# Performance work log

Measured on AMD Instinct MI355X. Metric: run time of the kernel, lower is better.

## Reference

```python
import jax, jax.numpy as jnp
import numpy as np

D_MODEL = 1024
NUM_HEADS = 16
D_K = D_MODEL // NUM_HEADS
THETA = 10000.0
MAX_SEQ_LEN = 4096


def setup_inputs() -> dict:
    key = jax.random.key(0)
    ks = jax.random.split(key, 5)
    scale = 1.0 / np.sqrt(D_MODEL)
    x = jax.random.normal(ks[0], (2, 2048, D_MODEL), dtype=jnp.float32)
    wq = jax.random.normal(ks[1], (D_MODEL, D_MODEL), dtype=jnp.float32) * scale
    wk = jax.random.normal(ks[2], (D_MODEL, D_MODEL), dtype=jnp.float32) * scale
    wv = jax.random.normal(ks[3], (D_MODEL, D_MODEL), dtype=jnp.float32) * scale
    wo = jax.random.normal(ks[4], (D_MODEL, D_MODEL), dtype=jnp.float32) * scale
    return {"x": x, "wq": wq, "wk": wk, "wv": wv, "wo": wo}


def _rope(t, cos, sin):
    # t: (B, H, S, d_k) with interleaved even/odd pairs
    pairs = t.reshape(*t.shape[:-1], D_K // 2, 2)
    e, o = pairs[..., 0], pairs[..., 1]
    oe = e * cos - o * sin
    oo = e * sin + o * cos
    return jnp.stack([oe, oo], axis=-1).reshape(t.shape)


def reference(x, wq, wk, wv, wo):
    B, S, _ = x.shape
    # QKV projections (Linear: y = x @ W^T, no bias)
    def proj(w):
        y = jnp.einsum('bsd,ed->bse', x, w)
        return y.reshape(B, S, NUM_HEADS, D_K).transpose(0, 2, 1, 3)  # (B,H,S,dk)
    q, k, v = proj(wq), proj(wk), proj(wv)

    # RoPE angles for positions 0..S-1
    pair_idx = jnp.arange(0, D_K, 2, dtype=jnp.float32)
    inv_freq = 1.0 / (THETA ** (pair_idx / D_K))
    pos = jnp.arange(S, dtype=jnp.float32)
    ang = pos[:, None] * inv_freq[None, :]          # (S, dk/2)
    cos, sin = jnp.cos(ang), jnp.sin(ang)
    q = _rope(q, cos, sin)
    k = _rope(k, cos, sin)

    scores = jnp.einsum('bhqd,bhkd->bhqk', q, k) / jnp.sqrt(jnp.float32(D_K))
    causal = jnp.tril(jnp.ones((S, S), dtype=bool))
    scores = jnp.where(causal, scores, jnp.finfo(scores.dtype).min)
    attn = jax.nn.softmax(scores, axis=-1)
    out = jnp.einsum('bhqk,bhkd->bhqd', attn, v)    # (B,H,S,dk)
    out = out.transpose(0, 2, 1, 3).reshape(B, S, D_MODEL)
    return jnp.einsum('bsd,ed->bse', out, wo)
```

## Files before the change

kernel.cpp:

```cpp
#include <hip/hip_runtime.h>
#include <hip/hip_bf16.h>
#include <stdint.h>

#define S_LEN  2048
#define DMODEL 1024
#define NHEADS 16
#define DKH    64
#define NBATCH 2
#define NROWS  (NBATCH * S_LEN)
#define NBH    (NBATCH * NHEADS)
#define KVS    72

typedef unsigned short ushort_t;
typedef __attribute__((ext_vector_type(8))) short bf16x8;
typedef __attribute__((ext_vector_type(4))) float f32x4;
typedef __attribute__((ext_vector_type(4))) unsigned short us4;
typedef __attribute__((ext_vector_type(4))) unsigned int u32x4;

__device__ __forceinline__ ushort_t f2bf(float f) {
  union { float f; unsigned int u; } c; c.f = f;
  unsigned int r = c.u + 0x7FFFu + ((c.u >> 16) & 1u);
  return (ushort_t)(r >> 16);
}

__device__ __forceinline__ unsigned int pack_bf16(float lo, float hi) {
  union { __hip_bfloat162 h; unsigned int u; } cv;
  cv.h = __float22bfloat162_rn(make_float2(lo, hi));
  return cv.u;
}

__device__ __forceinline__ void gload_lds16(const void* g, void* l) {
  __builtin_amdgcn_global_load_lds((const __attribute__((address_space(1))) void*)g,
                                   (__attribute__((address_space(3))) void*)l, 16, 0, 0);
}

__global__ void cast5_kernel(const float* __restrict__ x,
                             const float* __restrict__ a, const float* __restrict__ b,
                             const float* __restrict__ c, const float* __restrict__ d,
                             ushort_t* __restrict__ dst) {
  const int i = (blockIdx.x * 256 + threadIdx.x) * 4;
  const int sel = i >> 20;
  const float* src;
  int off;
  if (sel < 4)      { src = x; off = i; }
  else if (sel == 4){ src = a; off = i & ((1 << 20) - 1); }
  else if (sel == 5){ src = b; off = i & ((1 << 20) - 1); }
  else if (sel == 6){ src = c; off = i & ((1 << 20) - 1); }
  else              { src = d; off = i & ((1 << 20) - 1); }
  const float4 v = *(const float4*)(src + off);
  us4 o;
  o.x = f2bf(v.x); o.y = f2bf(v.y); o.z = f2bf(v.z); o.w = f2bf(v.w);
  *(us4*)(dst + i) = o;
}

template<int EPI>
__device__ __forceinline__ void gemm_core(const ushort_t* __restrict__ A, const ushort_t* __restrict__ Bm,
                                          void* __restrict__ Cp, void* __restrict__ Cp2,
                                          int N, int r0, int c0,
                                          ushort_t* As, ushort_t* Bs)
{
  const int tid  = threadIdx.x;
  const int lane = tid & 63;
  const int w    = tid >> 6;
  const int wr   = (w >> 1) * 64;
  const int wc   = (w & 1) * 64;
  const int g    = lane >> 4;
  const int lr   = lane & 15;
  const int K    = 1024;

  f32x4 acc[4][4] = {};

  const int idx0 = tid, idx1 = 256 + tid;
  const int row0 = idx0 >> 2, ce0 = (idx0 & 3) * 8;
  const int row1 = idx1 >> 2, ce1 = (idx1 & 3) * 8;

  for (int k0 = 0; k0 < K; k0 += 32) {
    gload_lds16(A  + (size_t)(r0 + row0) * K + k0 + ce0, As + idx0 * 8);
    gload_lds16(A  + (size_t)(r0 + row1) * K + k0 + ce1, As + idx1 * 8);
    gload_lds16(Bm + (size_t)(c0 + row0) * K + k0 + ce0, Bs + idx0 * 8);
    gload_lds16(Bm + (size_t)(c0 + row1) * K + k0 + ce1, Bs + idx1 * 8);
    __syncthreads();
    bf16x8 af[4], bfr[4];
    #pragma unroll
    for (int i = 0; i < 4; i++) {
      af[i]  = *(const bf16x8*)(As + (wr + i * 16 + lr) * 32 + g * 8);
      bfr[i] = *(const bf16x8*)(Bs + (wc + i * 16 + lr) * 32 + g * 8);
    }
    #pragma unroll
    for (int mf = 0; mf < 4; mf++)
      #pragma unroll
      for (int nf = 0; nf < 4; nf++)
        acc[mf][nf] = __builtin_amdgcn_mfma_f32_16x16x32_bf16(af[mf], bfr[nf], acc[mf][nf], 0, 0, 0);
    __syncthreads();
  }

  #pragma unroll
  for (int mf = 0; mf < 4; mf++) {
    #pragma unroll
    for (int nf = 0; nf < 4; nf++) {
      #pragma unroll
      for (int r = 0; r < 4; r++) {
        const int row = r0 + wr + mf * 16 + g * 4 + r;
        const int col = c0 + wc + nf * 16 + lr;
        float v = acc[mf][nf][r];
        if constexpr (EPI == 0) {
          ((ushort_t*)Cp)[(size_t)row * N + col] = f2bf(v);
        } else {
          float pv = __shfl_xor(v, 1);
          const int cc  = col & (DMODEL - 1);
          const int pos = row & (S_LEN - 1);
          const int d   = cc & (DKH - 1);
          const int pr  = d >> 1;
          const float inv = exp2f((float)pr * -0.41524100952f);
          const float ang = (float)pos * inv;
          float sn, cs;
          __sincosf(ang, &sn, &cs);
          float outv = (d & 1) ? (pv * sn + v * cs) : (v * cs - pv * sn);
          if (col < DMODEL) outv *= 0.125f;
          const int b = row >> 11, s = row & (S_LEN - 1);
          const int h = cc >> 6;
          ushort_t* dst = (ushort_t*)((col < DMODEL) ? Cp : Cp2);
          dst[(((size_t)(b * NHEADS + h)) * S_LEN + s) * DKH + d] = f2bf(outv);
        }
      }
    }
  }
}

__global__ __launch_bounds__(256, 2)
void proj_kernel(const ushort_t* __restrict__ xb, const ushort_t* __restrict__ wqb,
                 const ushort_t* __restrict__ wvb,
                 ushort_t* __restrict__ qb, ushort_t* __restrict__ kb, ushort_t* __restrict__ vtb)
{
  __shared__ ushort_t As[128 * 32];
  __shared__ ushort_t Bs[128 * 32];
  const int lin = (int)blockIdx.x;
  const int nl  = (lin & 7) * 96 + (lin >> 3);
  if (nl < 512) {
    gemm_core<2>(xb, wqb, qb, kb, 2 * DMODEL, (nl >> 4) * 128, (nl & 15) * 128, As, Bs);
  } else {
    const int m = nl - 512;
    gemm_core<0>(wvb, xb, vtb, nullptr, NROWS, (m >> 5) * 128, (m & 31) * 128, As, Bs);
  }
}

__global__ __launch_bounds__(256, 2)
void gemm_final(const ushort_t* __restrict__ A, const ushort_t* __restrict__ Bm,
                float* __restrict__ Cp)
{
  __shared__ ushort_t As[128 * 32];
  __shared__ ushort_t Bs[64 * 32];
  const int lin  = (int)blockIdx.x;
  const int nl   = (lin & 7) * 64 + (lin >> 3);
  const int r0   = (nl >> 4) * 128;
  const int c0   = (nl & 15) * 64;
  const int tid  = threadIdx.x;
  const int lane = tid & 63;
  const int w    = tid >> 6;
  const int wr   = (w >> 1) * 64;
  const int wc   = (w & 1) * 32;
  const int g    = lane >> 4;
  const int lr   = lane & 15;
  const int K    = 1024;

  f32x4 acc[4][2] = {};
  const int idx0 = tid, idx1 = 256 + tid;
  const int rowA0 = idx0 >> 2, ceA0 = (idx0 & 3) * 8;
  const int rowA1 = idx1 >> 2, ceA1 = (idx1 & 3) * 8;
  const int rowB  = tid >> 2,  ceB  = (tid & 3) * 8;

  for (int k0 = 0; k0 < K; k0 += 32) {
    gload_lds16(A  + (size_t)(r0 + rowA0) * K + k0 + ceA0, As + idx0 * 8);
    gload_lds16(A  + (size_t)(r0 + rowA1) * K + k0 + ceA1, As + idx1 * 8);
    gload_lds16(Bm + (size_t)(c0 + rowB) * K + k0 + ceB,  Bs + tid * 8);
    __syncthreads();
    bf16x8 af[4], bfr[2];
    #pragma unroll
    for (int i = 0; i < 4; i++)
      af[i] = *(const bf16x8*)(As + (wr + i * 16 + lr) * 32 + g * 8);
    #pragma unroll
    for (int i = 0; i < 2; i++)
      bfr[i] = *(const bf16x8*)(Bs + (wc + i * 16 + lr) * 32 + g * 8);
    #pragma unroll
    for (int mf = 0; mf < 4; mf++)
      #pragma unroll
      for (int nf = 0; nf < 2; nf++)
        acc[mf][nf] = __builtin_amdgcn_mfma_f32_16x16x32_bf16(af[mf], bfr[nf], acc[mf][nf], 0, 0, 0);
    __syncthreads();
  }
  #pragma unroll
  for (int mf = 0; mf < 4; mf++)
    #pragma unroll
    for (int nf = 0; nf < 2; nf++)
      #pragma unroll
      for (int r = 0; r < 4; r++) {
        const int row = r0 + wr + mf * 16 + g * 4 + r;
        const int col = c0 + wc + nf * 16 + lr;
        Cp[(size_t)row * DMODEL + col] = acc[mf][nf][r];
      }
}

__global__ __launch_bounds__(512, 4)
void attn_kernel(const ushort_t* __restrict__ Q, const ushort_t* __restrict__ Kh,
                 const ushort_t* __restrict__ VT, ushort_t* __restrict__ Out)
{
  __shared__ ushort_t Ks[2][64 * KVS];
  __shared__ ushort_t Vs[2][64 * KVS];
  const int tid  = threadIdx.x;
  const int lane = tid & 63;
  const int w    = tid >> 6;
  const int grp  = w >> 2;
  const int wid  = w & 3;
  const int g    = lane >> 4, lr = lane & 15;

  const int id = (int)blockIdx.x;
  const int bh = id & 31;
  const int qt = 31 - (id >> 5);
  const int b  = bh >> 4, h = bh & 15;

  const ushort_t* Kbase = Kh + (size_t)bh * S_LEN * DKH;
  const ushort_t* Vbase = VT + (size_t)h * DKH * (size_t)NROWS + (size_t)b * S_LEN;

  ushort_t* Ksg = &Ks[grp][0];
  ushort_t* Vsg = &Vs[grp][0];
  float* MB = (float*)&Ks[1][0];
  float* SB = MB + 64 * 68;

  const int tg   = tid & 255;
  const int krow = tg >> 3;
  const int kcol = (tg & 7) * 8;

  const int qrow = qt * 64 + wid * 16;

  bf16x8 qf0, qf1;
  {
    const ushort_t* qp = Q + ((size_t)bh * S_LEN + qrow + lr) * DKH;
    qf0 = *(const bf16x8*)(qp + g * 8);
    qf1 = *(const bf16x8*)(qp + 32 + g * 8);
  }
  f32x4 o[4] = {};
  float lsum = 0.f;

  bf16x8 kr0, kr1, vr0, vr1;
  if (grp <= qt) {
    const int kv0 = grp * 64;
    kr0 = *(const bf16x8*)(Kbase + (size_t)(kv0 + krow) * DKH + kcol);
    kr1 = *(const bf16x8*)(Kbase + (size_t)(kv0 + 32 + krow) * DKH + kcol);
    vr0 = *(const bf16x8*)(Vbase + (size_t)krow * NROWS + kv0 + kcol);
    vr1 = *(const bf16x8*)(Vbase + (size_t)(32 + krow) * NROWS + kv0 + kcol);
  }

  const int nT = qt / 2 + 1;
  for (int t = 0; t < nT; t++) {
    const int tk  = 2 * t + grp;
    const bool act = (tk <= qt);
    const bool pre = (tk + 2 <= qt);

    __syncthreads();
    if (act) {
      *(bf16x8*)(Ksg + krow * KVS + kcol) = kr0;
      *(bf16x8*)(Ksg + (32 + krow) * KVS + kcol) = kr1;
      *(bf16x8*)(Vsg + krow * KVS + kcol) = vr0;
      *(bf16x8*)(Vsg + (32 + krow) * KVS + kcol) = vr1;
    }
    __syncthreads();
    if (pre) {
      const int kv0n = (tk + 2) * 64;
      kr0 = *(const bf16x8*)(Kbase + (size_t)(kv0n + krow) * DKH + kcol);
      kr1 = *(const bf16x8*)(Kbase + (size_t)(kv0n + 32 + krow) * DKH + kcol);
      vr0 = *(const bf16x8*)(Vbase + (size_t)krow * NROWS + kv0n + kcol);
      vr1 = *(const bf16x8*)(Vbase + (size_t)(32 + krow) * NROWS + kv0n + kcol);
    }

    if (act) {
      f32x4 s4[4];
      __builtin_amdgcn_s_setprio(1);
      #pragma unroll
      for (int nf = 0; nf < 4; nf++) {
        bf16x8 b0 = *(const bf16x8*)(Ksg + (nf * 16 + lr) * KVS + g * 8);
        bf16x8 b1 = *(const bf16x8*)(Ksg + (nf * 16 + lr) * KVS + 32 + g * 8);
        f32x4 z = {};
        z = __builtin_amdgcn_mfma_f32_16x16x32_bf16(b0, qf0, z, 0, 0, 0);
        z = __builtin_amdgcn_mfma_f32_16x16x32_bf16(b1, qf1, z, 0, 0, 0);
        s4[nf] = z;
      }
      __builtin_amdgcn_s_setprio(0);

      if (tk == qt) {
        const int qg = qrow + lr;
        #pragma unroll
        for (int nf = 0; nf < 4; nf++) {
          const int kvb = tk * 64 + nf * 16 + g * 4;
          #pragma unroll
          for (int r = 0; r < 4; r++)
            if (kvb + r > qg) s4[nf][r] = -3.0e38f;
        }
      }

      float p[4][4];
      #pragma unroll
      for (int nf = 0; nf < 4; nf++)
        #pragma unroll
        for (int r = 0; r < 4; r++) p[nf][r] = __expf(s4[nf][r]);
      lsum += ((p[0][0] + p[0][1]) + (p[0][2] + p[0][3])) + ((p[1][0] + p[1][1]) + (p[1][2] + p[1][3]))
            + ((p[2][0] + p[2][1]) + (p[2][2] + p[2][3])) + ((p[3][0] + p[3][1]) + (p[3][2] + p[3][3]));

      bf16x8 pa[2];
      const int src0 = ((g & 1) << 5) + lr;
      const int src1 = src0 + 16;
      const bool xl = (g < 2);
      #pragma unroll
      for (int kf = 0; kf < 2; kf++) {
        const unsigned int x0 = pack_bf16(p[2 * kf][0], p[2 * kf][1]);
        const unsigned int x1 = pack_bf16(p[2 * kf][2], p[2 * kf][3]);
        const unsigned int y0 = pack_bf16(p[2 * kf + 1][0], p[2 * kf + 1][1]);
        const unsigned int y1 = pack_bf16(p[2 * kf + 1][2], p[2 * kf + 1][3]);
        const unsigned int a0 = (unsigned int)__shfl((int)x0, src0);
        const unsigned int b0 = (unsigned int)__shfl((int)y0, src0);
        const unsigned int a1 = (unsigned int)__shfl((int)x1, src0);
        const unsigned int b1 = (unsigned int)__shfl((int)y1, src0);
        const unsigned int a2 = (unsigned int)__shfl((int)x0, src1);
        const unsigned int b2 = (unsigned int)__shfl((int)y0, src1);
        const unsigned int a3 = (unsigned int)__shfl((int)x1, src1);
        const unsigned int b3 = (unsigned int)__shfl((int)y1, src1);
        u32x4 wds;
        wds.x = xl ? a0 : b0;
        wds.y = xl ? a1 : b1;
        wds.z = xl ? a2 : b2;
        wds.w = xl ? a3 : b3;
        pa[kf] = *(bf16x8*)&wds;
      }

      __builtin_amdgcn_s_setprio(1);
      #pragma unroll
      for (int kf = 0; kf < 2; kf++)
        #pragma unroll
        for (int nf = 0; nf < 4; nf++) {
          const bf16x8 vB = *(const bf16x8*)(Vsg + (nf * 16 + lr) * KVS + kf * 32 + g * 8);
          o[nf] = __builtin_amdgcn_mfma_f32_16x16x32_bf16(pa[kf], vB, o[nf], 0, 0, 0);
        }
      __builtin_amdgcn_s_setprio(0);
    }
  }

  lsum += __shfl_xor(lsum, 16);
  lsum += __shfl_xor(lsum, 32);

  __syncthreads();
  if (grp == 1) {
    #pragma unroll
    for (int nf = 0; nf < 4; nf++)
      #pragma unroll
      for (int r = 0; r < 4; r++)
        MB[(wid * 16 + g * 4 + r) * 68 + nf * 16 + lr] = o[nf][r];
    if (g == 0) SB[wid * 16 + lr] = lsum;
  }
  __syncthreads();
  if (grp == 0) {
    #pragma unroll
    for (int r = 0; r < 4; r++) {
      const int rl  = g * 4 + r;
      const int rho = wid * 16 + rl;
      const float lB = SB[rho];
      const float lA = __shfl(lsum, (lane & 48) | rl);
      const float inv = 1.0f / (lA + lB);
      const int s = qt * 64 + rho;
      #pragma unroll
      for (int nf = 0; nf < 4; nf++) {
        const float val = (o[nf][r] + MB[rho * 68 + nf * 16 + lr]) * inv;
        Out[((size_t)b * S_LEN + s) * DMODEL + h * DKH + nf * 16 + lr] = f2bf(val);
      }
    }
  }
}

extern "C" void kernel_launch(void* const* d_in, const int* in_sizes, int n_in,
                              void* d_out, int out_size, void* d_ws, size_t ws_size,
                              hipStream_t stream)
{
  const float* x  = (const float*)d_in[0];
  const float* wq = (const float*)d_in[1];
  const float* wk = (const float*)d_in[2];
  const float* wv = (const float*)d_in[3];
  const float* wo = (const float*)d_in[4];
  float* out = (float*)d_out;
  ushort_t* ws = (ushort_t*)d_ws;

  ushort_t* xb  = ws;
  ushort_t* wqb = xb  + (size_t)NROWS * DMODEL;
  ushort_t* wkb = wqb + (size_t)DMODEL * DMODEL;
  ushort_t* wvb = wkb + (size_t)DMODEL * DMODEL;
  ushort_t* wob = wvb + (size_t)DMODEL * DMODEL;
  ushort_t* qb  = wob + (size_t)DMODEL * DMODEL;
  ushort_t* kb  = qb  + (size_t)NROWS * DMODEL;
  ushort_t* vtb = kb  + (size_t)NROWS * DMODEL;
  ushort_t* ab  = xb;

  cast5_kernel<<<8192, 256, 0, stream>>>(x, wq, wk, wv, wo, ws);

  proj_kernel<<<768, 256, 0, stream>>>(xb, wqb, wvb, qb, kb, vtb);
  attn_kernel<<<1024, 512, 0, stream>>>(qb, kb, vtb, ab);
  gemm_final<<<512, 256, 0, stream>>>(ab, wob, out);
}
```

Measured before the change: 108.4 us.

## Process 128 query rows per attention block to reuse K/V tiles

Each attention block now covers a 128-row query tile instead of 64. Each wave computes two 16-row query sub-tiles against every K/V tile staged in shared memory, and the grid is halved. This reuses each staged K/V tile for twice as many queries, reducing global loads and barriers per unit of work. Fully masked sub-tiles are skipped with per-sub-tile live flags, and the block order is changed to interleave heavy and light query tiles. The cost is higher register pressure under the existing launch bounds, a two-pass epilogue, and fewer blocks to balance the causal workload.

```diff
diff --git a/kernel.cpp b/kernel.cpp
--- a/kernel.cpp
+++ b/kernel.cpp
@@ -215,7 +215,8 @@
 
   const int id = (int)blockIdx.x;
   const int bh = id & 31;
-  const int qt = 31 - (id >> 5);
+  const int u  = id >> 5;
+  const int qt = (u < 8) ? (15 - u) : (u - 8);
   const int b  = bh >> 4, h = bh & 15;
 
   const ushort_t* Kbase = Kh + (size_t)bh * S_LEN * DKH;
@@ -223,26 +224,27 @@
 
   ushort_t* Ksg = &Ks[grp][0];
   ushort_t* Vsg = &Vs[grp][0];
-  float* MB = (float*)&Ks[1][0];
+  float* MB = (float*)&Ks[0][0];
   float* SB = MB + 64 * 68;
 
   const int tg   = tid & 255;
   const int krow = tg >> 3;
   const int kcol = (tg & 7) * 8;
 
-  const int qrow = qt * 64 + wid * 16;
-
-  bf16x8 qf0, qf1;
+  const int qrow0 = qt * 128 + wid * 32;
+
+  bf16x8 qf[2][2];
+  #pragma unroll
+  for (int s = 0; s < 2; s++) {
+    const ushort_t* qp = Q + ((size_t)bh * S_LEN + qrow0 + s * 16 + lr) * DKH;
+    qf[s][0] = *(const bf16x8*)(qp + g * 8);
+    qf[s][1] = *(const bf16x8*)(qp + 32 + g * 8);
+  }
+  f32x4 o[2][4] = {};
+  float lsum[2] = {0.f, 0.f};
+
+  bf16x8 kr0, kr1, vr0, vr1;
   {
-    const ushort_t* qp = Q + ((size_t)bh * S_LEN + qrow + lr) * DKH;
-    qf0 = *(const bf16x8*)(qp + g * 8);
-    qf1 = *(const bf16x8*)(qp + 32 + g * 8);
-  }
-  f32x4 o[4] = {};
-  float lsum = 0.f;
-
-  bf16x8 kr0, kr1, vr0, vr1;
-  if (grp <= qt) {
     const int kv0 = grp * 64;
     kr0 = *(const bf16x8*)(Kbase + (size_t)(kv0 + krow) * DKH + kcol);
     kr1 = *(const bf16x8*)(Kbase + (size_t)(kv0 + 32 + krow) * DKH + kcol);
@@ -250,85 +252,94 @@
     vr1 = *(const bf16x8*)(Vbase + (size_t)(32 + krow) * NROWS + kv0 + kcol);
   }
 
-  const int nT = qt / 2 + 1;
+  const int nT = qt + 1;
   for (int t = 0; t < nT; t++) {
-    const int tk  = 2 * t + grp;
-    const bool act = (tk <= qt);
-    const bool pre = (tk + 2 <= qt);
-
-    __syncthreads();
-    if (act) {
-      *(bf16x8*)(Ksg + krow * KVS + kcol) = kr0;
-      *(bf16x8*)(Ksg + (32 + krow) * KVS + kcol) = kr1;
-      *(bf16x8*)(Vsg + krow * KVS + kcol) = vr0;
-      *(bf16x8*)(Vsg + (32 + krow) * KVS + kcol) = vr1;
-    }
-    __syncthreads();
-    if (pre) {
-      const int kv0n = (tk + 2) * 64;
-      kr0 = *(const bf16x8*)(Kbase + (size_t)(kv0n + krow) * DKH + kcol);
-      kr1 = *(const bf16x8*)(Kbase + (size_t)(kv0n + 32 + krow) * DKH + kcol);
-      vr0 = *(const bf16x8*)(Vbase + (size_t)krow * NROWS + kv0n + kcol);
-      vr1 = *(const bf16x8*)(Vbase + (size_t)(32 + krow) * NROWS + kv0n + kcol);
-    }
-
-    if (act) {
-      f32x4 s4[4];
+    const int kv0 = (2 * t + grp) * 64;
+    __syncthreads();
+    *(bf16x8*)(Ksg + krow * KVS + kcol) = kr0;
+    *(bf16x8*)(Ksg + (32 + krow) * KVS + kcol) = kr1;
+    *(bf16x8*)(Vsg + krow * KVS + kcol) = vr0;
+    *(bf16x8*)(Vsg + (32 + krow) * KVS + kcol) = vr1;
+    __syncthreads();
+    if (t < nT - 1) {
+      const int kvn = kv0 + 128;
+      kr0 = *(const bf16x8*)(Kbase + (size_t)(kvn + krow) * DKH + kcol);
+      kr1 = *(const bf16x8*)(Kbase + (size_t)(kvn + 32 + krow) * DKH + kcol);
+      vr0 = *(const bf16x8*)(Vbase + (size_t)krow * NROWS + kvn + kcol);
+      vr1 = *(const bf16x8*)(Vbase + (size_t)(32 + krow) * NROWS + kvn + kcol);
+    }
+
+    const bool live0 = (kv0 <= qrow0 + 15);
+    const bool live1 = (kv0 <= qrow0 + 31);
+    if (live1) {
+      f32x4 s4[2][4];
       __builtin_amdgcn_s_setprio(1);
       #pragma unroll
       for (int nf = 0; nf < 4; nf++) {
         bf16x8 b0 = *(const bf16x8*)(Ksg + (nf * 16 + lr) * KVS + g * 8);
         bf16x8 b1 = *(const bf16x8*)(Ksg + (nf * 16 + lr) * KVS + 32 + g * 8);
-        f32x4 z = {};
-        z = __builtin_amdgcn_mfma_f32_16x16x32_bf16(b0, qf0, z, 0, 0, 0);
-        z = __builtin_amdgcn_mfma_f32_16x16x32_bf16(b1, qf1, z, 0, 0, 0);
-        s4[nf] = z;
+        f32x4 z1 = {};
+        z1 = __builtin_amdgcn_mfma_f32_16x16x32_bf16(b0, qf[1][0], z1, 0, 0, 0);
+        z1 = __builtin_amdgcn_mfma_f32_16x16x32_bf16(b1, qf[1][1], z1, 0, 0, 0);
+        s4[1][nf] = z1;
+        if (live0) {
+          f32x4 z0 = {};
+          z0 = __builtin_amdgcn_mfma_f32_16x16x32_bf16(b0, qf[0][0], z0, 0, 0, 0);
+          z0 = __builtin_amdgcn_mfma_f32_16x16x32_bf16(b1, qf[0][1], z0, 0, 0, 0);
+          s4[0][nf] = z0;
+        }
       }
       __builtin_amdgcn_s_setprio(0);
 
-      if (tk == qt) {
-        const int qg = qrow + lr;
-        #pragma unroll
-        for (int nf = 0; nf < 4; nf++) {
-          const int kvb = tk * 64 + nf * 16 + g * 4;
+      bf16x8 pa[2][2];
+      #pragma unroll
+      for (int s = 0; s < 2; s++) {
+        const bool lv = s ? live1 : live0;
+        if (lv) {
+          const int qrS = qrow0 + s * 16;
+          if (kv0 + 63 > qrS) {
+            const int qg = qrS + lr;
+            #pragma unroll
+            for (int nf = 0; nf < 4; nf++) {
+              const int kvb = kv0 + nf * 16 + g * 4;
+              #pragma unroll
+              for (int r = 0; r < 4; r++)
+                if (kvb + r > qg) s4[s][nf][r] = -3.0e38f;
+            }
+          }
+          float p[4][4];
           #pragma unroll
-          for (int r = 0; r < 4; r++)
-            if (kvb + r > qg) s4[nf][r] = -3.0e38f;
+          for (int nf = 0; nf < 4; nf++)
+            #pragma unroll
+            for (int r = 0; r < 4; r++) p[nf][r] = __expf(s4[s][nf][r]);
+          lsum[s] += ((p[0][0] + p[0][1]) + (p[0][2] + p[0][3])) + ((p[1][0] + p[1][1]) + (p[1][2] + p[1][3]))
+                   + ((p[2][0] + p[2][1]) + (p[2][2] + p[2][3])) + ((p[3][0] + p[3][1]) + (p[3][2] + p[3][3]));
+
+          const int src0 = ((g & 1) << 5) + lr;
+          const int src1 = src0 + 16;
+          const bool xl = (g < 2);
+          #pragma unroll
+          for (int kf = 0; kf < 2; kf++) {
+            const unsigned int x0 = pack_bf16(p[2 * kf][0], p[2 * kf][1]);
+            const unsigned int x1 = pack_bf16(p[2 * kf][2], p[2 * kf][3]);
+            const unsigned int y0 = pack_bf16(p[2 * kf + 1][0], p[2 * kf + 1][1]);
+            const unsigned int y1 = pack_bf16(p[2 * kf + 1][2], p[2 * kf + 1][3]);
+            const unsigned int a0 = (unsigned int)__shfl((int)x0, src0);
+            const unsigned int b0 = (unsigned int)__shfl((int)y0, src0);
+            const unsigned int a1 = (unsigned int)__shfl((int)x1, src0);
+            const unsigned int b1 = (unsigned int)__shfl((int)y1, src0);
+            const unsigned int a2 = (unsigned int)__shfl((int)x0, src1);
+            const unsigned int b2 = (unsigned int)__shfl((int)y0, src1);
+            const unsigned int a3 = (unsigned int)__shfl((int)x1, src1);
+            const unsigned int b3 = (unsigned int)__shfl((int)y1, src1);
+            u32x4 wds;
+            wds.x = xl ? a0 : b0;
+            wds.y = xl ? a1 : b1;
+            wds.z = xl ? a2 : b2;
+            wds.w = xl ? a3 : b3;
+            pa[s][kf] = *(bf16x8*)&wds;
+          }
         }
-      }
-
-      float p[4][4];
-      #pragma unroll
-      for (int nf = 0; nf < 4; nf++)
-        #pragma unroll
-        for (int r = 0; r < 4; r++) p[nf][r] = __expf(s4[nf][r]);
-      lsum += ((p[0][0] + p[0][1]) + (p[0][2] + p[0][3])) + ((p[1][0] + p[1][1]) + (p[1][2] + p[1][3]))
-            + ((p[2][0] + p[2][1]) + (p[2][2] + p[2][3])) + ((p[3][0] + p[3][1]) + (p[3][2] + p[3][3]));
-
-      bf16x8 pa[2];
-      const int src0 = ((g & 1) << 5) + lr;
-      const int src1 = src0 + 16;
-      const bool xl = (g < 2);
-      #pragma unroll
-      for (int kf = 0; kf < 2; kf++) {
-        const unsigned int x0 = pack_bf16(p[2 * kf][0], p[2 * kf][1]);
-        const unsigned int x1 = pack_bf16(p[2 * kf][2], p[2 * kf][3]);
-        const unsigned int y0 = pack_bf16(p[2 * kf + 1][0], p[2 * kf + 1][1]);
-        const unsigned int y1 = pack_bf16(p[2 * kf + 1][2], p[2 * kf + 1][3]);
-        const unsigned int a0 = (unsigned int)__shfl((int)x0, src0);
-        const unsigned int b0 = (unsigned int)__shfl((int)y0, src0);
-        const unsigned int a1 = (unsigned int)__shfl((int)x1, src0);
-        const unsigned int b1 = (unsigned int)__shfl((int)y1, src0);
-        const unsigned int a2 = (unsigned int)__shfl((int)x0, src1);
-        const unsigned int b2 = (unsigned int)__shfl((int)y0, src1);
-        const unsigned int a3 = (unsigned int)__shfl((int)x1, src1);
-        const unsigned int b3 = (unsigned int)__shfl((int)y1, src1);
-        u32x4 wds;
-        wds.x = xl ? a0 : b0;
-        wds.y = xl ? a1 : b1;
-        wds.z = xl ? a2 : b2;
-        wds.w = xl ? a3 : b3;
-        pa[kf] = *(bf16x8*)&wds;
       }
 
       __builtin_amdgcn_s_setprio(1);
@@ -337,38 +348,53 @@
         #pragma unroll
         for (int nf = 0; nf < 4; nf++) {
           const bf16x8 vB = *(const bf16x8*)(Vsg + (nf * 16 + lr) * KVS + kf * 32 + g * 8);
-          o[nf] = __builtin_amdgcn_mfma_f32_16x16x32_bf16(pa[kf], vB, o[nf], 0, 0, 0);
+          if (live0) o[0][nf] = __builtin_amdgcn_mfma_f32_16x16x32_bf16(pa[0][kf], vB, o[0][nf], 0, 0, 0);
+          o[1][nf] = __builtin_amdgcn_mfma_f32_16x16x32_bf16(pa[1][kf], vB, o[1][nf], 0, 0, 0);
         }
       __builtin_amdgcn_s_setprio(0);
     }
   }
 
-  lsum += __shfl_xor(lsum, 16);
-  lsum += __shfl_xor(lsum, 32);
-
-  __syncthreads();
-  if (grp == 1) {
-    #pragma unroll
-    for (int nf = 0; nf < 4; nf++)
-      #pragma unroll
-      for (int r = 0; r < 4; r++)
-        MB[(wid * 16 + g * 4 + r) * 68 + nf * 16 + lr] = o[nf][r];
-    if (g == 0) SB[wid * 16 + lr] = lsum;
-  }
-  __syncthreads();
-  if (grp == 0) {
-    #pragma unroll
-    for (int r = 0; r < 4; r++) {
-      const int rl  = g * 4 + r;
-      const int rho = wid * 16 + rl;
-      const float lB = SB[rho];
-      const float lA = __shfl(lsum, (lane & 48) | rl);
-      const float inv = 1.0f / (lA + lB);
-      const int s = qt * 64 + rho;
-      #pragma unroll
-      for (int nf = 0; nf < 4; nf++) {
-        const float val = (o[nf][r] + MB[rho * 68 + nf * 16 + lr]) * inv;
-        Out[((size_t)b * S_LEN + s) * DMODEL + h * DKH + nf * 16 + lr] = f2bf(val);
+  #pragma unroll
+  for (int s = 0; s < 2; s++) {
+    lsum[s] += __shfl_xor(lsum[s], 16);
+    lsum[s] += __shfl_xor(lsum[s], 32);
+  }
+
+  const int hw    = wid >> 1;
+  const int rbase = (wid & 1) * 32;
+  #pragma unroll
+  for (int hh = 0; hh < 2; hh++) {
+    __syncthreads();
+    if (grp == 1 && hw == hh) {
+      #pragma unroll
+      for (int s = 0; s < 2; s++) {
+        #pragma unroll
+        for (int nf = 0; nf < 4; nf++)
+          #pragma unroll
+          for (int r = 0; r < 4; r++)
+            MB[(rbase + s * 16 + g * 4 + r) * 68 + nf * 16 + lr] = o[s][nf][r];
+        if (g == 0) SB[rbase + s * 16 + lr] = lsum[s];
+      }
+    }
+    __syncthreads();
+    if (grp == 0 && hw == hh) {
+      #pragma unroll
+      for (int s = 0; s < 2; s++) {
+        #pragma unroll
+        for (int r = 0; r < 4; r++) {
+          const int rl  = g * 4 + r;
+          const int rho = rbase + s * 16 + rl;
+          const float lB = SB[rho];
+          const float lA = __shfl(lsum[s], (lane & 48) | rl);
+          const float inv = 1.0f / (lA + lB);
+          const int sg = qt * 128 + hh * 64 + rho;
+          #pragma unroll
+          for (int nf = 0; nf < 4; nf++) {
+            const float val = (o[s][nf][r] + MB[rho * 68 + nf * 16 + lr]) * inv;
+            Out[((size_t)b * S_LEN + sg) * DMODEL + h * DKH + nf * 16 + lr] = f2bf(val);
+          }
+        }
       }
     }
   }
@@ -399,6 +425,6 @@
   cast5_kernel<<<8192, 256, 0, stream>>>(x, wq, wk, wv, wo, ws);
 
   proj_kernel<<<768, 256, 0, stream>>>(xb, wqb, wvb, qb, kb, vtb);
-  attn_kernel<<<1024, 512, 0, stream>>>(qb, kb, vtb, ab);
+  attn_kernel<<<512, 512, 0, stream>>>(qb, kb, vtb, ab);
   gemm_final<<<512, 256, 0, stream>>>(ab, wob, out);
 }
```

Result: slower. 152.8 us (+41.0%).
